# Performance work log

Hardware: AMD Instinct MI355X
Metric: run time of the kernel (lower is better)

## Reference

```python
import jax, jax.numpy as jnp
import numpy as np

B, L, D, H = 2, 2048, 512, 8
SAMPLING_FACTOR = 5


def setup_inputs() -> dict:
    key = jax.random.key(0)
    ks = jax.random.split(key, 12)
    L_K = min(8000, L)
    log_L_K = int(np.ceil(np.log1p(L_K)))
    U_part = min(SAMPLING_FACTOR * L * log_L_K, L_K)  # = 2048
    inp = {
        'q': jax.random.normal(ks[0], (B, L, D), jnp.float32),
        'k': jax.random.normal(ks[1], (B, L, D), jnp.float32),
        'v': jax.random.normal(ks[2], (B, L, D), jnp.float32),
        'Wq': jax.random.normal(ks[3], (D, D), jnp.float32) * 0.02,
        'bq': jnp.zeros((D,), jnp.float32),
        'Wk': jax.random.normal(ks[4], (D, D), jnp.float32) * 0.02,
        'bk': jnp.zeros((D,), jnp.float32),
        'Wv': jax.random.normal(ks[5], (D, D), jnp.float32) * 0.02,
        'bv': jnp.zeros((D,), jnp.float32),
        'Wo': jax.random.normal(ks[6], (D, D), jnp.float32) * 0.02,
        'bo': jnp.zeros((D,), jnp.float32),
        'index_sample': jax.random.randint(ks[7], (U_part,), 0, L_K, jnp.int32),
    }
    return inp


def _prob_sparse(qh, Kh, Vh, index_sample):
    # qh, Kh, Vh: [B, H, L, d]
    L_K = min(8000, Kh.shape[2])  # K_sample = K[:, :8000]; L_K = its length
    L_Q = qh.shape[2]
    Ks = Kh[:, :, index_sample, :]                                  # [B,H,U,d]
    QKs = jnp.einsum('bhqd,bhkd->bhqk', qh, Ks)                     # [B,H,Lq,U]
    # M = max - sum/L_K  (source divides by L_K, not U_part)
    M = QKs.max(axis=-1) - QKs.sum(axis=-1) / L_K                   # [B,H,Lq]
    u = min(SAMPLING_FACTOR * int(np.ceil(np.log1p(L_Q))), L_Q)     # = 40
    _, M_top = jax.lax.top_k(-M, u)                                 # topk(largest=False)
    Q_red = jnp.take_along_axis(qh, M_top[..., None], axis=2)       # [B,H,u,d]
    d_k = qh.shape[-1]
    scores = jnp.einsum('bhqd,bhkd->bhqk', Q_red, Kh) / jnp.sqrt(jnp.asarray(d_k, qh.dtype))
    probs = jax.nn.softmax(scores, axis=-1)
    out = jnp.einsum('bhqk,bhkd->bhqd', probs, Vh)                  # [B,H,u,d]
    return out, scores


def reference(q, k, v, Wq, bq, Wk, bk, Wv, bv, Wo, bo, index_sample):
    qp = q @ Wq.T + bq
    kp = k @ Wk.T + bk
    vp = v @ Wv.T + bv
    Bsz, Lq, Dm = qp.shape
    d = Dm // H
    # faithful to source: q is view'd to [B,H,Lq,d] WITHOUT transpose
    qh = qp.reshape(Bsz, H, Lq, d)
    kh = kp.reshape(Bsz, -1, H, d).transpose(0, 2, 1, 3)
    vh = vp.reshape(Bsz, -1, H, d).transpose(0, 2, 1, 3)
    out, _ = _prob_sparse(qh, kh, vh, index_sample)
    u = out.shape[2]
    out = out.transpose(0, 2, 1, 3).reshape(Bsz, u, Dm)             # concat
    return out @ Wo.T + bo                                          # [B,u,D]
```

## Files before the change

### kernel.cpp

```cpp
#include <hip/hip_runtime.h>
#include <math.h>

#define B_ 2
#define L_ 2048
#define D_ 512
#define H_ 8
#define DH 64
#define NS 2048
#define NU 40
#define BHD (L_*D_)
#define QHS (L_*DH)

typedef __attribute__((ext_vector_type(8))) short bf16x8;
typedef __attribute__((ext_vector_type(4))) float f32x4;

__device__ inline float4 ld4(const float* p) { return *reinterpret_cast<const float4*>(p); }

__device__ inline unsigned short hi16(float x) { return (unsigned short)(__float_as_uint(x) >> 16); }
__device__ inline float trunchf(float x) { return __uint_as_float(__float_as_uint(x) & 0xFFFF0000u); }
__device__ inline void tsplit(float x, unsigned short& hs, unsigned short& ms, unsigned short& ls) {
  float h = trunchf(x); hs = hi16(x);
  float r = x - h;
  float m = trunchf(r); ms = hi16(r);
  float r2 = r - m;
  ls = hi16(r2);
}

__global__ __launch_bounds__(256) void proj_mfma(
    const float* __restrict__ qa, const float* __restrict__ ka, const float* __restrict__ va,
    const float* __restrict__ Wq, const float* __restrict__ Wk, const float* __restrict__ Wv,
    const float* __restrict__ bq, const float* __restrict__ bk, const float* __restrict__ bv,
    float* __restrict__ qp, float* __restrict__ kp, float* __restrict__ vp)
{
  __shared__ __align__(16) unsigned short a3[3][128][36];
  __shared__ __align__(16) unsigned short w3[3][128][36];
  const int t = threadIdx.x;
  const int mat = blockIdx.z;
  const float* A    = (mat == 0) ? qa : (mat == 1) ? ka : va;
  const float* W    = (mat == 0) ? Wq : (mat == 1) ? Wk : Wv;
  const float* bias = (mat == 0) ? bq : (mat == 1) ? bk : bv;
  float* C          = (mat == 0) ? qp : (mat == 1) ? kp : vp;
  const int m0 = blockIdx.x * 128, n0 = blockIdx.y * 128;
  const int w = t >> 6, l = t & 63;
  const int wm = w >> 1, wn = w & 1;
  const int lr = l & 15, lg = l >> 4;
  const int srow = t >> 1, sc0 = (t & 1) * 16;

  f32x4 acc[4][4];
#pragma unroll
  for (int i = 0; i < 4; ++i)
#pragma unroll
    for (int j = 0; j < 4; ++j) acc[i][j] = (f32x4){0.f, 0.f, 0.f, 0.f};

  for (int kc = 0; kc < 16; ++kc) {
    const int kb = kc * 32;
    __syncthreads();
    {
      const float* src = A + (size_t)(m0 + srow) * 512 + kb + sc0;
      float xs[16];
#pragma unroll
      for (int i = 0; i < 4; ++i) {
        float4 v4 = ld4(src + 4*i);
        xs[4*i] = v4.x; xs[4*i+1] = v4.y; xs[4*i+2] = v4.z; xs[4*i+3] = v4.w;
      }
#pragma unroll
      for (int hh = 0; hh < 2; ++hh) {
        union { bf16x8 v; unsigned short u[8]; } H, M, L;
#pragma unroll
        for (int e = 0; e < 8; ++e) tsplit(xs[hh*8 + e], H.u[e], M.u[e], L.u[e]);
        *reinterpret_cast<bf16x8*>(&a3[0][srow][sc0 + 8*hh]) = H.v;
        *reinterpret_cast<bf16x8*>(&a3[1][srow][sc0 + 8*hh]) = M.v;
        *reinterpret_cast<bf16x8*>(&a3[2][srow][sc0 + 8*hh]) = L.v;
      }
    }
    {
      const float* src = W + (size_t)(n0 + srow) * 512 + kb + sc0;
      float xs[16];
#pragma unroll
      for (int i = 0; i < 4; ++i) {
        float4 v4 = ld4(src + 4*i);
        xs[4*i] = v4.x; xs[4*i+1] = v4.y; xs[4*i+2] = v4.z; xs[4*i+3] = v4.w;
      }
#pragma unroll
      for (int hh = 0; hh < 2; ++hh) {
        union { bf16x8 v; unsigned short u[8]; } H, M, L;
#pragma unroll
        for (int e = 0; e < 8; ++e) tsplit(xs[hh*8 + e], H.u[e], M.u[e], L.u[e]);
        *reinterpret_cast<bf16x8*>(&w3[0][srow][sc0 + 8*hh]) = H.v;
        *reinterpret_cast<bf16x8*>(&w3[1][srow][sc0 + 8*hh]) = M.v;
        *reinterpret_cast<bf16x8*>(&w3[2][srow][sc0 + 8*hh]) = L.v;
      }
    }
    __syncthreads();

    bf16x8 af[3][4], bf[3][4];
#pragma unroll
    for (int p = 0; p < 3; ++p)
#pragma unroll
      for (int mi = 0; mi < 4; ++mi)
        af[p][mi] = *reinterpret_cast<const bf16x8*>(&a3[p][wm*64 + mi*16 + lr][lg*8]);
#pragma unroll
    for (int p = 0; p < 3; ++p)
#pragma unroll
      for (int ni = 0; ni < 4; ++ni)
        bf[p][ni] = *reinterpret_cast<const bf16x8*>(&w3[p][wn*64 + ni*16 + lr][lg*8]);
#pragma unroll
    for (int mi = 0; mi < 4; ++mi)
#pragma unroll
      for (int ni = 0; ni < 4; ++ni) {
        acc[mi][ni] = __builtin_amdgcn_mfma_f32_16x16x32_bf16(af[0][mi], bf[0][ni], acc[mi][ni], 0, 0, 0);
        acc[mi][ni] = __builtin_amdgcn_mfma_f32_16x16x32_bf16(af[0][mi], bf[1][ni], acc[mi][ni], 0, 0, 0);
        acc[mi][ni] = __builtin_amdgcn_mfma_f32_16x16x32_bf16(af[1][mi], bf[0][ni], acc[mi][ni], 0, 0, 0);
        acc[mi][ni] = __builtin_amdgcn_mfma_f32_16x16x32_bf16(af[1][mi], bf[1][ni], acc[mi][ni], 0, 0, 0);
        acc[mi][ni] = __builtin_amdgcn_mfma_f32_16x16x32_bf16(af[0][mi], bf[2][ni], acc[mi][ni], 0, 0, 0);
        acc[mi][ni] = __builtin_amdgcn_mfma_f32_16x16x32_bf16(af[2][mi], bf[0][ni], acc[mi][ni], 0, 0, 0);
      }
  }
#pragma unroll
  for (int mi = 0; mi < 4; ++mi)
#pragma unroll
    for (int ni = 0; ni < 4; ++ni) {
      const int gn = n0 + wn*64 + ni*16 + lr;
      const float bv_ = bias[gn];
#pragma unroll
      for (int r = 0; r < 4; ++r) {
        const int gm = m0 + wm*64 + mi*16 + lg*4 + r;
        C[(size_t)gm * 512 + gn] = acc[mi][ni][r] + bv_;
      }
    }
}

__global__ __launch_bounds__(1024) void ksum_kernel(const float* __restrict__ kp,
                                                    const int* __restrict__ idx,
                                                    float* __restrict__ ksum) {
  __shared__ float part[16][64];
  const int bh = blockIdx.x;
  const int b = bh >> 3, h = bh & 7;
  const int t = threadIdx.x;
  const int sg = t >> 6, j = t & 63;
  const float* kbase = kp + (size_t)b*BHD + h*DH;
  float a = 0.f;
  for (int s = sg*128; s < sg*128 + 128; ++s)
    a += kbase[(size_t)idx[s]*512 + j];
  part[sg][j] = a;
  __syncthreads();
  if (t < 64) {
    float s = 0.f;
#pragma unroll
    for (int i = 0; i < 16; ++i) s += part[i][t];
    ksum[bh*64 + t] = s;
  }
}

__global__ __launch_bounds__(256) void m_kernel(const float* __restrict__ qp,
                                                const float* __restrict__ kp,
                                                const int* __restrict__ idx,
                                                float* __restrict__ Mp) {
  __shared__ __align__(16) unsigned short k3[3][128][72];
  const int t = threadIdx.x;
  const int bid = blockIdx.x;
  const int bh = bid >> 4, qt = (bid >> 1) & 7, ks = bid & 1;
  const int b = bh >> 3, h = bh & 7;
  const int w = t >> 6, l = t & 63;
  const int lr = l & 15;
  const int lg = l >> 4;

  bf16x8 qf[4][2][3];
  {
    const float* qbase = qp + (size_t)b*BHD + (size_t)h*QHS + (size_t)(qt*256 + w*64 + lr) * 64 + lg*8;
#pragma unroll
    for (int mi = 0; mi < 4; ++mi)
#pragma unroll
      for (int c = 0; c < 2; ++c) {
        const float* src = qbase + mi*16*64 + c*32;
        float4 x0 = ld4(src), x1 = ld4(src + 4);
        float xs[8] = {x0.x, x0.y, x0.z, x0.w, x1.x, x1.y, x1.z, x1.w};
        union { bf16x8 v; unsigned short u[8]; } H, M, L;
#pragma unroll
        for (int e = 0; e < 8; ++e) tsplit(xs[e], H.u[e], M.u[e], L.u[e]);
        qf[mi][c][0] = H.v; qf[mi][c][1] = M.v; qf[mi][c][2] = L.v;
      }
  }

  const float* kbase = kp + (size_t)b*BHD + h*DH;
  const int ib = ks * 1024;
  const int srow = t >> 1, sh = (t & 1) * 32;

  float4 vst[8];
  {
    const int kr = idx[ib + srow];
    const float* src = kbase + (size_t)kr * 512 + sh;
#pragma unroll
    for (int i = 0; i < 8; ++i) vst[i] = ld4(src + 4*i);
  }

  float mx[4][4];
#pragma unroll
  for (int mi = 0; mi < 4; ++mi)
#pragma unroll
    for (int r = 0; r < 4; ++r) mx[mi][r] = -INFINITY;

  for (int tl = 0; tl < 8; ++tl) {
    __syncthreads();
    {
#pragma unroll
      for (int e2 = 0; e2 < 4; ++e2) {
        union { bf16x8 v; unsigned short u[8]; } H, M, L;
        float xs[8] = {vst[2*e2].x, vst[2*e2].y, vst[2*e2].z, vst[2*e2].w,
                       vst[2*e2+1].x, vst[2*e2+1].y, vst[2*e2+1].z, vst[2*e2+1].w};
#pragma unroll
        for (int e = 0; e < 8; ++e) tsplit(xs[e], H.u[e], M.u[e], L.u[e]);
        *reinterpret_cast<bf16x8*>(&k3[0][srow][sh + 8*e2]) = H.v;
        *reinterpret_cast<bf16x8*>(&k3[1][srow][sh + 8*e2]) = M.v;
        *reinterpret_cast<bf16x8*>(&k3[2][srow][sh + 8*e2]) = L.v;
      }
    }
    if (tl < 7) {
      const int kr = idx[ib + (tl+1)*128 + srow];
      const float* src = kbase + (size_t)kr * 512 + sh;
#pragma unroll
      for (int i = 0; i < 8; ++i) vst[i] = ld4(src + 4*i);
    }
    __syncthreads();

    for (int n2 = 0; n2 < 4; ++n2) {
      bf16x8 bf[2][3][2];
#pragma unroll
      for (int ns = 0; ns < 2; ++ns)
#pragma unroll
        for (int p = 0; p < 3; ++p)
#pragma unroll
          for (int c = 0; c < 2; ++c)
            bf[ns][p][c] = *reinterpret_cast<const bf16x8*>(&k3[p][n2*32 + ns*16 + lr][c*32 + lg*8]);
#pragma unroll
      for (int mi = 0; mi < 4; ++mi)
#pragma unroll
        for (int ns = 0; ns < 2; ++ns) {
          f32x4 acc = {0.f, 0.f, 0.f, 0.f};
#pragma unroll
          for (int c = 0; c < 2; ++c) acc = __builtin_amdgcn_mfma_f32_16x16x32_bf16(qf[mi][c][0], bf[ns][0][c], acc, 0, 0, 0);
#pragma unroll
          for (int c = 0; c < 2; ++c) acc = __builtin_amdgcn_mfma_f32_16x16x32_bf16(qf[mi][c][0], bf[ns][1][c], acc, 0, 0, 0);
#pragma unroll
          for (int c = 0; c < 2; ++c) acc = __builtin_amdgcn_mfma_f32_16x16x32_bf16(qf[mi][c][1], bf[ns][0][c], acc, 0, 0, 0);
#pragma unroll
          for (int c = 0; c < 2; ++c) acc = __builtin_amdgcn_mfma_f32_16x16x32_bf16(qf[mi][c][1], bf[ns][1][c], acc, 0, 0, 0);
#pragma unroll
          for (int c = 0; c < 2; ++c) acc = __builtin_amdgcn_mfma_f32_16x16x32_bf16(qf[mi][c][0], bf[ns][2][c], acc, 0, 0, 0);
#pragma unroll
          for (int c = 0; c < 2; ++c) acc = __builtin_amdgcn_mfma_f32_16x16x32_bf16(qf[mi][c][2], bf[ns][0][c], acc, 0, 0, 0);
#pragma unroll
          for (int r = 0; r < 4; ++r) mx[mi][r] = fmaxf(mx[mi][r], acc[r]);
        }
    }
  }

#pragma unroll
  for (int mi = 0; mi < 4; ++mi)
#pragma unroll
    for (int r = 0; r < 4; ++r) {
      float v = mx[mi][r];
      v = fmaxf(v, __shfl_xor(v, 1));
      v = fmaxf(v, __shfl_xor(v, 2));
      v = fmaxf(v, __shfl_xor(v, 4));
      v = fmaxf(v, __shfl_xor(v, 8));
      if (lr == 0)
        Mp[ks*32768 + bh*2048 + qt*256 + w*64 + mi*16 + lg*4 + r] = v;
    }
}

__global__ __launch_bounds__(256) void topk_kernel(const float* __restrict__ qp,
                                                   const float* __restrict__ ksum,
                                                   const float* __restrict__ Mp,
                                                   int* __restrict__ Mtop) {
  __shared__ float mv[2048];
  __shared__ float ks_s[64];
  __shared__ float wvs[4];
  __shared__ int   wis[4];
  const int bh = blockIdx.x;
  const int b = bh >> 3, h = bh & 7;
  const int t = threadIdx.x;
  if (t < 64) ks_s[t] = ksum[bh*64 + t];
  __syncthreads();
#pragma unroll
  for (int c = 0; c < 8; ++c) {
    const int qi = c * 256 + t;
    const float* qrow = qp + (size_t)b*BHD + (size_t)h*QHS + (size_t)qi * 64;
    float dot = 0.f;
#pragma unroll
    for (int cc = 0; cc < 16; ++cc) {
      float4 q4 = ld4(qrow + 4 * cc);
      dot += q4.x * ks_s[4*cc + 0];
      dot += q4.y * ks_s[4*cc + 1];
      dot += q4.z * ks_s[4*cc + 2];
      dot += q4.w * ks_s[4*cc + 3];
    }
    mv[qi] = fmaxf(Mp[bh*2048 + qi], Mp[32768 + bh*2048 + qi]) - dot * (1.0f/2048.0f);
  }
  __syncthreads();
  const int wl = t & 63, w = t >> 6;
  for (int it = 0; it < NU; ++it) {
    float bv = mv[t]; int bi = t;
#pragma unroll
    for (int c = 1; c < 8; ++c) {
      const float v = mv[t + 256*c];
      if (v < bv) { bv = v; bi = t + 256*c; }
    }
#pragma unroll
    for (int off = 1; off < 64; off <<= 1) {
      const float ov = __shfl_xor(bv, off);
      const int   oi = __shfl_xor(bi, off);
      if (ov < bv || (ov == bv && oi < bi)) { bv = ov; bi = oi; }
    }
    if (wl == 0) { wvs[w] = bv; wis[w] = bi; }
    __syncthreads();
    if (t == 0) {
      float fv = wvs[0]; int fi = wis[0];
#pragma unroll
      for (int w2 = 1; w2 < 4; ++w2)
        if (wvs[w2] < fv || (wvs[w2] == fv && wis[w2] < fi)) { fv = wvs[w2]; fi = wis[w2]; }
      Mtop[bh*NU + it] = fi;
      mv[fi] = INFINITY;
    }
    __syncthreads();
  }
}

__global__ __launch_bounds__(256) void flash_partial(const float* __restrict__ qp,
                                                     const float* __restrict__ kp,
                                                     const float* __restrict__ vp,
                                                     const int* __restrict__ Mtop,
                                                     float* __restrict__ pm,
                                                     float* __restrict__ pl,
                                                     float* __restrict__ pacc) {
  __shared__ float qr[NU][65];
  __shared__ float kv[64][65];
  __shared__ float sl[NU][65];
  __shared__ float ms[NU], ls[NU], fs[NU];
  const int bid = blockIdx.x;
  const int bh = bid >> 4, kt = bid & 15;
  const int b = bh >> 3, h = bh & 7;
  const int t = threadIdx.x;
  const int g = t >> 6, j = t & 63;
  const int r4 = t >> 2, sub = t & 3;

  {
    const float* qbase = qp + (size_t)b*BHD + (size_t)h*QHS;
#pragma unroll
    for (int r = 0; r < 10; ++r) {
      const int q = g*10 + r;
      qr[q][j] = qbase[(size_t)Mtop[bh*NU + q]*64 + j];
    }
  }
  if (t < NU) { ms[t] = -INFINITY; ls[t] = 0.f; }
  float acc[10];
#pragma unroll
  for (int r = 0; r < 10; ++r) acc[r] = 0.f;

  const float* kbase = kp + (size_t)b*BHD + h*DH;
  const float* vbase = vp + (size_t)b*BHD + h*DH;
  const int srow = t >> 2, scb = (t & 3)*16;

  for (int st = 0; st < 2; ++st) {
    const int kb = kt*128 + st*64;
    __syncthreads();
    {
      const float* src = kbase + (size_t)(kb + srow)*512 + scb;
#pragma unroll
      for (int i = 0; i < 4; ++i) {
        float4 v = ld4(src + 4*i);
        kv[srow][scb + 4*i + 0] = v.x;
        kv[srow][scb + 4*i + 1] = v.y;
        kv[srow][scb + 4*i + 2] = v.z;
        kv[srow][scb + 4*i + 3] = v.w;
      }
    }
    __syncthreads();
    {
      float sv[10];
#pragma unroll
      for (int r = 0; r < 10; ++r) {
        const int q = g*10 + r;
        float s = 0.f;
#pragma unroll 8
        for (int jj = 0; jj < 64; ++jj) s += qr[q][jj]*kv[j][jj];
        sv[r] = s * 0.125f;
      }
#pragma unroll
      for (int r = 0; r < 10; ++r) sl[g*10 + r][j] = sv[r];
    }
    __syncthreads();
    float4 vst[4];
    {
      const float* src = vbase + (size_t)(kb + srow)*512 + scb;
#pragma unroll
      for (int i = 0; i < 4; ++i) vst[i] = ld4(src + 4*i);
    }
    if (r4 < NU) {
      float tm = -INFINITY;
#pragma unroll
      for (int c = 0; c < 16; ++c) tm = fmaxf(tm, sl[r4][sub*16 + c]);
      tm = fmaxf(tm, __shfl_xor(tm, 1));
      tm = fmaxf(tm, __shfl_xor(tm, 2));
      const float nm = fmaxf(ms[r4], tm);
      if (sub == 0) { fs[r4] = expf(ms[r4] - nm); ms[r4] = nm; }
    }
    __syncthreads();
    {
#pragma unroll
      for (int r = 0; r < 10; ++r) {
        const int q = g*10 + r;
        acc[r] *= fs[q];
        sl[q][j] = expf(sl[q][j] - ms[q]);
      }
#pragma unroll
      for (int i = 0; i < 4; ++i) {
        kv[srow][scb + 4*i + 0] = vst[i].x;
        kv[srow][scb + 4*i + 1] = vst[i].y;
        kv[srow][scb + 4*i + 2] = vst[i].z;
        kv[srow][scb + 4*i + 3] = vst[i].w;
      }
    }
    __syncthreads();
    if (r4 < NU) {
      float s = 0.f;
#pragma unroll
      for (int c = 0; c < 16; ++c) s += sl[r4][sub*16 + c];
      s += __shfl_xor(s, 1);
      s += __shfl_xor(s, 2);
      if (sub == 0) ls[r4] = ls[r4]*fs[r4] + s;
    }
    {
#pragma unroll 4
      for (int kk = 0; kk < 64; ++kk) {
        const float vv = kv[kk][j];
#pragma unroll
        for (int r = 0; r < 10; ++r) acc[r] += sl[g*10 + r][kk]*vv;
      }
    }
  }
  __syncthreads();
  const size_t base = (size_t)(bh*16 + kt)*NU;
  if (t < NU) { pm[base + t] = ms[t]; pl[base + t] = ls[t]; }
#pragma unroll
  for (int r = 0; r < 10; ++r)
    pacc[(base + g*10 + r)*64 + j] = acc[r];
}

__global__ __launch_bounds__(256) void flash_combine(const float* __restrict__ pm,
                                                     const float* __restrict__ pl,
                                                     const float* __restrict__ pacc,
                                                     float* __restrict__ outc) {
  const int t = threadIdx.x;
  const int qg = t >> 6, j = t & 63;
  const int bh = blockIdx.x / 10;
  const int q  = (blockIdx.x % 10)*4 + qg;
  const int b = bh >> 3, h = bh & 7;
  float m = -INFINITY;
#pragma unroll
  for (int kt = 0; kt < 16; ++kt) m = fmaxf(m, pm[(size_t)(bh*16 + kt)*NU + q]);
  float Lsum = 0.f, num = 0.f;
#pragma unroll
  for (int kt = 0; kt < 16; ++kt) {
    const size_t base = (size_t)(bh*16 + kt)*NU;
    const float w = expf(pm[base + q] - m);
    Lsum += w * pl[base + q];
    num  += w * pacc[(base + q)*64 + j];
  }
  outc[(size_t)(b*NU + q)*512 + h*64 + j] = num / Lsum;
}

__global__ __launch_bounds__(256) void wo_gemm(const float* __restrict__ outc,
                                               const float* __restrict__ Wo,
                                               float* __restrict__ pwo) {
  __shared__ __align__(16) float a_t[80][68];
  __shared__ __align__(16) float w_t[64][68];
  const int t = threadIdx.x;
  const int ty = t >> 4, tx = t & 15;
  const int nt = blockIdx.x, ks = blockIdx.y;
  float acc[5][4];
#pragma unroll
  for (int i = 0; i < 5; ++i)
#pragma unroll
    for (int j = 0; j < 4; ++j) acc[i][j] = 0.f;

  for (int c = 0; c < 2; ++c) {
    const int kb = ks*128 + c*64;
    __syncthreads();
#pragma unroll
    for (int i = 0; i < 20; ++i) {
      const int fi = t + 256*i;
      const int row = fi >> 6, col = fi & 63;
      a_t[row][col] = outc[(size_t)row*512 + kb + col];
    }
#pragma unroll
    for (int i = 0; i < 16; ++i) {
      const int fi = t + 256*i;
      const int row = fi >> 6, col = fi & 63;
      w_t[row][col] = Wo[(size_t)(nt*64 + row)*512 + kb + col];
    }
    __syncthreads();
    for (int gq = 0; gq < 16; ++gq) {
      float4 av[5], wv[4];
#pragma unroll
      for (int i = 0; i < 5; ++i) av[i] = *reinterpret_cast<const float4*>(&a_t[ty + 16*i][4*gq]);
#pragma unroll
      for (int j = 0; j < 4; ++j) wv[j] = *reinterpret_cast<const float4*>(&w_t[tx + 16*j][4*gq]);
#pragma unroll
      for (int i = 0; i < 5; ++i)
#pragma unroll
        for (int j = 0; j < 4; ++j) {
          acc[i][j] += av[i].x * wv[j].x;
          acc[i][j] += av[i].y * wv[j].y;
          acc[i][j] += av[i].z * wv[j].z;
          acc[i][j] += av[i].w * wv[j].w;
        }
    }
  }
#pragma unroll
  for (int i = 0; i < 5; ++i)
#pragma unroll
    for (int j = 0; j < 4; ++j)
      pwo[ks*40960 + (size_t)(ty + 16*i)*512 + nt*64 + tx + 16*j] = acc[i][j];
}

__global__ __launch_bounds__(256) void wo_combine(const float* __restrict__ pwo,
                                                  const float* __restrict__ bo,
                                                  float* __restrict__ out) {
  const int gi = blockIdx.x*256 + threadIdx.x;
  const float4* p = reinterpret_cast<const float4*>(pwo);
  const float4 a = p[gi], b4 = p[10240 + gi], c4 = p[20480 + gi], d4 = p[30720 + gi];
  const float4 bb = ld4(bo + 4*(gi & 127));
  float4 o;
  o.x = a.x + b4.x + c4.x + d4.x + bb.x;
  o.y = a.y + b4.y + c4.y + d4.y + bb.y;
  o.z = a.z + b4.z + c4.z + d4.z + bb.z;
  o.w = a.w + b4.w + c4.w + d4.w + bb.w;
  reinterpret_cast<float4*>(out)[gi] = o;
}

extern "C" void kernel_launch(void* const* d_in, const int* in_sizes, int n_in,
                              void* d_out, int out_size, void* d_ws, size_t ws_size,
                              hipStream_t stream) {
  const float* q  = (const float*)d_in[0];
  const float* k  = (const float*)d_in[1];
  const float* v  = (const float*)d_in[2];
  const float* Wq = (const float*)d_in[3];
  const float* bq = (const float*)d_in[4];
  const float* Wk = (const float*)d_in[5];
  const float* bk = (const float*)d_in[6];
  const float* Wv = (const float*)d_in[7];
  const float* bv = (const float*)d_in[8];
  const float* Wo = (const float*)d_in[9];
  const float* bo = (const float*)d_in[10];
  const int*  idx = (const int*)d_in[11];

  float* ws   = (float*)d_ws;
  float* qp   = ws;
  float* kp   = ws + 2097152;
  float* vp   = ws + 4194304;
  float* ksum = ws + 6291456;
  int*   Mtop = (int*)(ws + 6292480);
  float* pm   = ws + 6293120;
  float* pl   = ws + 6303360;
  float* pacc = ws + 6313600;
  float* outc = ws + 6968960;
  float* Mp   = pm;
  float* pwo  = pm;

  const dim3 blk(256);
  proj_mfma<<<dim3(32, 4, 3), blk, 0, stream>>>(q, k, v, Wq, Wk, Wv, bq, bk, bv, qp, kp, vp);
  ksum_kernel<<<dim3(16), dim3(1024), 0, stream>>>(kp, idx, ksum);
  m_kernel<<<dim3(256), blk, 0, stream>>>(qp, kp, idx, Mp);
  topk_kernel<<<dim3(16), blk, 0, stream>>>(qp, ksum, Mp, Mtop);
  flash_partial<<<dim3(256), blk, 0, stream>>>(qp, kp, vp, Mtop, pm, pl, pacc);
  flash_combine<<<dim3(160), blk, 0, stream>>>(pm, pl, pacc, outc);
  wo_gemm<<<dim3(8, 4), blk, 0, stream>>>(outc, Wo, pwo);
  wo_combine<<<dim3(40), blk, 0, stream>>>(pwo, bo, (float*)d_out);
}
```

Before: 226.5 us.

## Replace iterative argmin top-k with radix-select threshold and rank sort

The top-k kernel previously ran 40 rounds of block-wide argmin, each with two barriers. It now turns each M value into an order-preserving unsigned key and finds the 40th-smallest key with a 4-pass 8-bit radix histogram select. Keys below the threshold are gathered with an atomic counter, and ties are filled in index order from a bitmap. The 40 results are then ranked within one wavefront to write sorted indices. This removes most barriers and serial iterations, at the cost of shared-memory atomics and a serial tie-fill done by one thread.

After: 199.1 us. -12.1%, faster.

```diff
diff --git a/kernel.cpp b/kernel.cpp
--- a/kernel.cpp
+++ b/kernel.cpp
@@ -273,15 +273,19 @@
                                                    const float* __restrict__ ksum,
                                                    const float* __restrict__ Mp,
                                                    int* __restrict__ Mtop) {
-  __shared__ float mv[2048];
   __shared__ float ks_s[64];
-  __shared__ float wvs[4];
-  __shared__ int   wis[4];
+  __shared__ unsigned hist[256];
+  __shared__ int wsum[4];
+  __shared__ unsigned bitmap[64];
+  __shared__ unsigned long long comb[NU];
+  __shared__ int s_sel, s_rem, s_cnt;
   const int bh = blockIdx.x;
   const int b = bh >> 3, h = bh & 7;
   const int t = threadIdx.x;
   if (t < 64) ks_s[t] = ksum[bh*64 + t];
   __syncthreads();
+
+  unsigned mykey[8];
 #pragma unroll
   for (int c = 0; c < 8; ++c) {
     const int qi = c * 256 + t;
@@ -295,34 +299,83 @@
       dot += q4.z * ks_s[4*cc + 2];
       dot += q4.w * ks_s[4*cc + 3];
     }
-    mv[qi] = fmaxf(Mp[bh*2048 + qi], Mp[32768 + bh*2048 + qi]) - dot * (1.0f/2048.0f);
-  }
+    const float m = fmaxf(Mp[bh*2048 + qi], Mp[32768 + bh*2048 + qi]) - dot * (1.0f/2048.0f);
+    const unsigned u = __float_as_uint(m);
+    mykey[c] = (u >> 31) ? ~u : (u | 0x80000000u);
+  }
+
+  unsigned prefMask = 0u, prefVal = 0u;
+  int rem = NU;
+  for (int shift = 24; shift >= 0; shift -= 8) {
+    hist[t] = 0;
+    __syncthreads();
+#pragma unroll
+    for (int c = 0; c < 8; ++c) {
+      const unsigned key = mykey[c];
+      if ((key & prefMask) == prefVal)
+        atomicAdd(&hist[(key >> shift) & 255], 1u);
+    }
+    __syncthreads();
+    const int binc = (int)hist[t];
+    int inc = binc;
+#pragma unroll
+    for (int off = 1; off < 64; off <<= 1) {
+      const int nb = __shfl_up(inc, off);
+      if ((t & 63) >= off) inc += nb;
+    }
+    if ((t & 63) == 63) wsum[t >> 6] = inc;
+    __syncthreads();
+    int wadd = 0;
+    for (int w2 = 0; w2 < (t >> 6); ++w2) wadd += wsum[w2];
+    const int incl = inc + wadd;
+    const int excl = incl - binc;
+    if (excl < rem && rem <= incl) { s_sel = t; s_rem = rem - excl; }
+    __syncthreads();
+    prefVal |= ((unsigned)s_sel) << shift;
+    prefMask |= 0xFFu << shift;
+    rem = s_rem;
+    __syncthreads();
+  }
+  const unsigned T = prefVal;
+
+  if (t < 64) bitmap[t] = 0;
+  if (t == 0) s_cnt = 0;
   __syncthreads();
-  const int wl = t & 63, w = t >> 6;
-  for (int it = 0; it < NU; ++it) {
-    float bv = mv[t]; int bi = t;
-#pragma unroll
-    for (int c = 1; c < 8; ++c) {
-      const float v = mv[t + 256*c];
-      if (v < bv) { bv = v; bi = t + 256*c; }
-    }
-#pragma unroll
-    for (int off = 1; off < 64; off <<= 1) {
-      const float ov = __shfl_xor(bv, off);
-      const int   oi = __shfl_xor(bi, off);
-      if (ov < bv || (ov == bv && oi < bi)) { bv = ov; bi = oi; }
-    }
-    if (wl == 0) { wvs[w] = bv; wis[w] = bi; }
-    __syncthreads();
-    if (t == 0) {
-      float fv = wvs[0]; int fi = wis[0];
-#pragma unroll
-      for (int w2 = 1; w2 < 4; ++w2)
-        if (wvs[w2] < fv || (wvs[w2] == fv && wis[w2] < fi)) { fv = wvs[w2]; fi = wis[w2]; }
-      Mtop[bh*NU + it] = fi;
-      mv[fi] = INFINITY;
-    }
-    __syncthreads();
+#pragma unroll
+  for (int c = 0; c < 8; ++c) {
+    const unsigned key = mykey[c];
+    const int qi = c * 256 + t;
+    if (key < T) {
+      const int pos = atomicAdd(&s_cnt, 1);
+      comb[pos] = ((unsigned long long)key << 11) | (unsigned)qi;
+    } else if (key == T) {
+      atomicOr(&bitmap[qi >> 5], 1u << (qi & 31));
+    }
+  }
+  __syncthreads();
+  if (t == 0) {
+    int need = rem, cpos = s_cnt;
+    for (int wd = 0; wd < 64 && need > 0; ++wd) {
+      unsigned bits = bitmap[wd];
+      while (bits && need > 0) {
+        const int bit = __ffs(bits) - 1;
+        bits &= bits - 1;
+        comb[cpos++] = ((unsigned long long)T << 11) | (unsigned)(wd*32 + bit);
+        --need;
+      }
+    }
+  }
+  __syncthreads();
+
+  if (t < 64) {
+    const unsigned long long mine = (t < NU) ? comb[t] : ~0ULL;
+    int rank = 0;
+#pragma unroll
+    for (int step = 1; step < 64; ++step) {
+      const unsigned long long other = __shfl(mine, (t + step) & 63);
+      rank += (other < mine) ? 1 : 0;
+    }
+    if (t < NU) Mtop[bh*NU + rank] = (int)(mine & 0x7FFu);
   }
 }
 
```
